# Optimization experiments

Measured on AMD Instinct MI355X. Metric: run time of the kernel, lower is better.

The kernel has to match this reference:

```python
import jax, jax.numpy as jnp
import numpy as np
import math

S, B, D = 1024, 8, 512
H = 8
HD = D // H
DFF = 2048
NUM_BUCKETS = 32
MAX_DISTANCE = 128
LN_EPS = 1e-5


def setup_inputs() -> dict:
    key = jax.random.key(0)
    ks = jax.random.split(key, 12)
    s = 0.02
    return {
        "x": jax.random.normal(ks[0], (S, B, D), jnp.float32),
        "attn_mask": jnp.zeros((S, S), jnp.float32),
        "in_proj_w": jax.random.normal(ks[1], (3 * D, D), jnp.float32) * s,
        "in_proj_b": jnp.zeros((3 * D,), jnp.float32),
        "out_proj_w": jax.random.normal(ks[2], (D, D), jnp.float32) * s,
        "out_proj_b": jnp.zeros((D,), jnp.float32),
        "lin1_w": jax.random.normal(ks[3], (DFF, D), jnp.float32) * s,
        "lin1_b": jnp.zeros((DFF,), jnp.float32),
        "lin2_w": jax.random.normal(ks[4], (D, DFF), jnp.float32) * s,
        "lin2_b": jnp.zeros((D,), jnp.float32),
        "ln1_w": jnp.ones((D,), jnp.float32),
        "ln1_b": jnp.zeros((D,), jnp.float32),
        "ln2_w": jnp.ones((D,), jnp.float32),
        "ln2_b": jnp.zeros((D,), jnp.float32),
        "rel_emb": jax.random.normal(ks[5], (NUM_BUCKETS, H), jnp.float32) * s,
    }


def _relative_position_bucket(relative_position, num_buckets=NUM_BUCKETS, max_distance=MAX_DISTANCE):
    # bidirectional=True path (encoder)
    nb = num_buckets // 2
    rel_buckets = (relative_position > 0).astype(jnp.int32) * nb
    rp = jnp.abs(relative_position)
    max_exact = nb // 2
    is_small = rp < max_exact
    rp_safe = jnp.maximum(rp, 1)  # avoid log(0); masked by is_small below
    rp_large = max_exact + (
        jnp.log(rp_safe.astype(jnp.float32) / max_exact)
        / math.log(max_distance / max_exact)
        * (nb - max_exact)
    ).astype(jnp.int32)
    rp_large = jnp.minimum(rp_large, nb - 1)
    return rel_buckets + jnp.where(is_small, rp, rp_large)


def _compute_bias(rel_emb, q_len, k_len):
    ctx = jnp.arange(q_len, dtype=jnp.int32)[:, None]
    mem = jnp.arange(k_len, dtype=jnp.int32)[None, :]
    buckets = _relative_position_bucket(mem - ctx)          # [S, S]
    values = rel_emb[buckets]                                # [S, S, H]
    return jnp.transpose(values, (2, 0, 1))                  # [H, S, S]


def _layer_norm(x, w, b):
    mu = jnp.mean(x, axis=-1, keepdims=True)
    var = jnp.mean(jnp.square(x - mu), axis=-1, keepdims=True)
    return (x - mu) * jax.lax.rsqrt(var + LN_EPS) * w + b


def reference(x, attn_mask, in_proj_w, in_proj_b, out_proj_w, out_proj_b,
              lin1_w, lin1_b, lin2_w, lin2_b, ln1_w, ln1_b, ln2_w, ln2_b, rel_emb):
    s, b, d = x.shape
    # qkv projection (torch Linear: y = x W^T + b)
    qkv = x @ in_proj_w.T + in_proj_b                         # [S, B, 3D]
    q, k, v = jnp.split(qkv, 3, axis=-1)

    def to_bhsd(t):
        return jnp.transpose(t.reshape(s, b, H, HD), (1, 2, 0, 3))  # [B, H, S, HD]

    q, k, v = to_bhsd(q), to_bhsd(k), to_bhsd(v)
    scores = jnp.einsum("bhqd,bhkd->bhqk", q, k) / math.sqrt(HD)

    bias = _compute_bias(rel_emb, s, s)                       # [H, S, S]
    mask_bias = attn_mask[None, :, :] + bias                  # [H, S, S]
    attn = jax.nn.softmax(scores + mask_bias[None], axis=-1)  # [B, H, S, S]

    o = jnp.einsum("bhqk,bhkd->bhqd", attn, v)                # [B, H, S, HD]
    o = jnp.transpose(o, (2, 0, 1, 3)).reshape(s, b, d)       # [S, B, D]
    o = o @ out_proj_w.T + out_proj_b

    # post-norm (norm_first=False)
    y = _layer_norm(x + o, ln1_w, ln1_b)
    ff = jax.nn.relu(y @ lin1_w.T + lin1_b) @ lin2_w.T + lin2_b
    return _layer_norm(y + ff, ln2_w, ln2_b)
```

## Files before the change

kernel.cpp:

```cpp
#include <hip/hip_runtime.h>
#include <hip/hip_bf16.h>


#define S_LEN 1024
#define BATCH 8
#define DMODEL 512
#define NHEAD 8
#define HDIM 64
#define DFF 2048
#define NROWS (S_LEN * BATCH)

typedef __bf16 bf16x8 __attribute__((ext_vector_type(8)));
typedef short  s16x4  __attribute__((ext_vector_type(4)));
typedef float  f32x4  __attribute__((ext_vector_type(4)));

__device__ __forceinline__ void gload16(const void* g, void* l) {
    __builtin_amdgcn_global_load_lds(
        (const __attribute__((address_space(1))) void*)g,
        (__attribute__((address_space(3))) void*)l, 16, 0, 0);
}

__global__ __launch_bounds__(256)
void prep_embc_kernel(const float* __restrict__ x,
                      const float* __restrict__ wq, const float* __restrict__ wo,
                      const float* __restrict__ w1, const float* __restrict__ w2,
                      __hip_bfloat16* __restrict__ xb, __hip_bfloat16* __restrict__ wqb,
                      __hip_bfloat16* __restrict__ wob, __hip_bfloat16* __restrict__ w1b,
                      __hip_bfloat16* __restrict__ w2b,
                      const float* __restrict__ mask,
                      const float* __restrict__ rel_emb,
                      __hip_bfloat16* __restrict__ embC) {
    if (blockIdx.x < 7168) {
        const int NX = NROWS * DMODEL / 4;
        const int NQ = 3 * DMODEL * DMODEL / 4;
        const int NO = DMODEL * DMODEL / 4;
        const int N1 = DFF * DMODEL / 4;
        int i = blockIdx.x * 256 + threadIdx.x;
        const float* src; __hip_bfloat16* dst; int off;
        if (i < NX)                         { src = x;  dst = xb;  off = i; }
        else if ((i -= NX) < NQ)            { src = wq; dst = wqb; off = i; }
        else if ((i -= NQ) < NO)            { src = wo; dst = wob; off = i; }
        else if ((i -= NO) < N1)            { src = w1; dst = w1b; off = i; }
        else if ((i -= N1) < N1)            { src = w2; dst = w2b; off = i; }
        else return;
        float4 v = *(const float4*)(src + (size_t)off * 4);
        union { s16x4 s; __hip_bfloat16 b[4]; } u;
        u.b[0] = __float2bfloat16(v.x); u.b[1] = __float2bfloat16(v.y);
        u.b[2] = __float2bfloat16(v.z); u.b[3] = __float2bfloat16(v.w);
        *(s16x4*)(dst + (size_t)off * 4) = u.s;
    } else {
        int tid = (blockIdx.x - 7168) * 256 + threadIdx.x;
        int h  = tid >> 16;
        int r1 = tid & 65535;
        int qt = r1 >> 12;
        int w  = (r1 >> 10) & 3;
        int kb = (r1 >> 6) & 15;
        int lane = r1 & 63;
        int q = qt * 64 + w * 16 + (lane & 15);
        __hip_bfloat16 ov[16];
#pragma unroll
        for (int j = 0; j < 16; ++j) {
            int c = j >> 2, e = j & 3;
            int k = kb * 64 + c * 16 + (lane >> 4) * 4 + e;
            int rel = k - q;
            int bucket = (rel > 0) ? 16 : 0;
            int rp = rel < 0 ? -rel : rel;
            int v;
            if (rp < 8)          v = rp;
            else if (rp < 12)    v = 8;
            else if (rp < 16)    v = 9;
            else if (rp < 23)    v = 10;
            else if (rp < 32)    v = 11;
            else if (rp < 46)    v = 12;
            else if (rp < 64)    v = 13;
            else if (rp < 91)    v = 14;
            else                 v = 15;
            float bt = rel_emb[(bucket + v) * NHEAD + h];
            ov[j] = __float2bfloat16(__expf(mask[(size_t)q * S_LEN + k] + bt));
        }
        *(uint4*)(embC + (size_t)tid * 16) = *(uint4*)&ov[0];
        *(uint4*)(embC + (size_t)tid * 16 + 8) = *(uint4*)&ov[8];
    }
}

template <int MODE, bool RELU>
__global__ __launch_bounds__(256)
void gemm_tile(const __hip_bfloat16* __restrict__ Ab,
               const __hip_bfloat16* __restrict__ Wb,
               const float* __restrict__ bias,
               void* __restrict__ outv,
               int N, int M, int Kloop, int Kstride) {
    const int id = blockIdx.x;
    int by, bx, bz;
    if (MODE == 0) { bz = id >> 8; int rem = id & 255; by = rem & 63; bx = rem >> 6; }
    else           { bz = 0; by = id & 63; bx = id >> 6; }
    const int w = threadIdx.x >> 6;
    const int lane = threadIdx.x & 63;
    const int m16 = lane & 15;
    const int quad = lane >> 4;
    const int row0 = by * 128;
    const int col0 = bx * 128;
    const int kbase = bz * Kloop;
    const int rowbase = (w >> 1) * 64;
    const int colbase = (w & 1) * 64;

    __shared__ __align__(16) __bf16 As[128 * 64];
    __shared__ __align__(16) __bf16 Bs[128 * 64];

    const __bf16* Ap = (const __bf16*)Ab;
    const __bf16* Wp = (const __bf16*)Wb;

    const int a_row_in_grp = lane >> 3;
    const int kb_sw = (lane & 7) ^ (lane >> 3);

    f32x4 acc[4][4];
#pragma unroll
    for (int c = 0; c < 4; ++c)
#pragma unroll
        for (int r = 0; r < 4; ++r) acc[c][r] = f32x4{0, 0, 0, 0};

    for (int k0 = 0; k0 < Kloop; k0 += 64) {
#pragma unroll
        for (int i = 0; i < 4; ++i) {
            int grp = w * 4 + i;
            int row = grp * 8 + a_row_in_grp;
            gload16(Ap + (size_t)(row0 + row) * Kstride + kbase + k0 + kb_sw * 8,
                    (void*)(As + grp * 512));
            gload16(Wp + (size_t)(col0 + row) * Kstride + kbase + k0 + kb_sw * 8,
                    (void*)(Bs + grp * 512));
        }
        __syncthreads();

#pragma unroll
        for (int kk = 0; kk < 2; ++kk) {
            bf16x8 af[4], bfr[4];
            int slot = (kk * 4 + quad) ^ (m16 & 7);
#pragma unroll
            for (int r = 0; r < 4; ++r)
                af[r] = *(const bf16x8*)(As + (rowbase + r * 16 + m16) * 64 + slot * 8);
#pragma unroll
            for (int c = 0; c < 4; ++c)
                bfr[c] = *(const bf16x8*)(Bs + (colbase + c * 16 + m16) * 64 + slot * 8);
#pragma unroll
            for (int c = 0; c < 4; ++c)
#pragma unroll
                for (int r = 0; r < 4; ++r)
                    acc[c][r] = __builtin_amdgcn_mfma_f32_16x16x32_bf16(
                        af[r], bfr[c], acc[c][r], 0, 0, 0);
        }
        __syncthreads();
    }

#pragma unroll
    for (int c = 0; c < 4; ++c) {
        int col = col0 + colbase + c * 16 + m16;
        float bv = (MODE == 0 && bz != 0) ? 0.f : bias[col];
#pragma unroll
        for (int r = 0; r < 4; ++r) {
#pragma unroll
            for (int e = 0; e < 4; ++e) {
                int row = row0 + rowbase + r * 16 + quad * 4 + e;
                float v = acc[c][r][e] + bv;
                if (RELU) v = fmaxf(v, 0.f);
                if (MODE == 0) {
                    ((float*)outv)[(size_t)bz * N * M + (size_t)row * M + col] = v;
                } else if (MODE == 1) {
                    ((__hip_bfloat16*)outv)[(size_t)row * M + col] = __float2bfloat16(v);
                } else {
                    int sect = col >> 9, h = (col >> 6) & 7, d = col & 63;
                    int s = row >> 3, bb = row & 7;
                    size_t idx;
                    if (sect == 2)
                        idx = (size_t)(128 + bb * 8 + h) * (S_LEN * HDIM)
                            + (size_t)d * S_LEN + s;
                    else
                        idx = ((size_t)(sect * 64 + bb * 8 + h) * S_LEN + s) * HDIM + d;
                    ((__hip_bfloat16*)outv)[idx] = __float2bfloat16(v);
                }
            }
        }
    }
}

__global__ __launch_bounds__(256)
void gemm64_db(const __hip_bfloat16* __restrict__ Ab,
               const __hip_bfloat16* __restrict__ Wb,
               const float* __restrict__ bias,
               float* __restrict__ outf,
               int N, int M, int K) {
    const int id = blockIdx.x;
    const int by = id & 63, bx = id >> 6;
    const int w = threadIdx.x >> 6;
    const int lane = threadIdx.x & 63;
    const int m16 = lane & 15;
    const int quad = lane >> 4;
    const int row0 = by * 128;
    const int col0 = bx * 64;
    const int rowbase = w * 32;

    __shared__ __align__(16) __bf16 As[2][128 * 64];
    __shared__ __align__(16) __bf16 Bs[2][64 * 64];

    const __bf16* Ap = (const __bf16*)Ab;
    const __bf16* Wp = (const __bf16*)Wb;

    const int a_row_in_grp = lane >> 3;
    const int kb_sw = (lane & 7) ^ (lane >> 3);

    auto stage = [&](int k0, int p) {
#pragma unroll
        for (int i = 0; i < 4; ++i) {
            int grp = w * 4 + i;
            int row = grp * 8 + a_row_in_grp;
            gload16(Ap + (size_t)(row0 + row) * K + k0 + kb_sw * 8,
                    (void*)(&As[p][grp * 512]));
        }
#pragma unroll
        for (int i = 0; i < 2; ++i) {
            int grp = w * 2 + i;
            int row = grp * 8 + a_row_in_grp;
            gload16(Wp + (size_t)(col0 + row) * K + k0 + kb_sw * 8,
                    (void*)(&Bs[p][grp * 512]));
        }
    };

    f32x4 acc[4][2];
#pragma unroll
    for (int c = 0; c < 4; ++c)
#pragma unroll
        for (int r = 0; r < 2; ++r) acc[c][r] = f32x4{0, 0, 0, 0};

    stage(0, 0);
    __syncthreads();

    int p = 0;
    for (int k0 = 0; k0 < K; k0 += 64, p ^= 1) {
        if (k0 + 64 < K) stage(k0 + 64, p ^ 1);
#pragma unroll
        for (int kk = 0; kk < 2; ++kk) {
            bf16x8 af[2], bfr[4];
            int slot = (kk * 4 + quad) ^ (m16 & 7);
#pragma unroll
            for (int r = 0; r < 2; ++r)
                af[r] = *(const bf16x8*)(&As[p][(rowbase + r * 16 + m16) * 64 + slot * 8]);
#pragma unroll
            for (int c = 0; c < 4; ++c)
                bfr[c] = *(const bf16x8*)(&Bs[p][(c * 16 + m16) * 64 + slot * 8]);
#pragma unroll
            for (int c = 0; c < 4; ++c)
#pragma unroll
                for (int r = 0; r < 2; ++r)
                    acc[c][r] = __builtin_amdgcn_mfma_f32_16x16x32_bf16(
                        af[r], bfr[c], acc[c][r], 0, 0, 0);
        }
        __syncthreads();
    }

#pragma unroll
    for (int c = 0; c < 4; ++c) {
        int col = col0 + c * 16 + m16;
        float bv = bias[col];
#pragma unroll
        for (int r = 0; r < 2; ++r)
#pragma unroll
            for (int e = 0; e < 4; ++e) {
                int row = row0 + rowbase + r * 16 + quad * 4 + e;
                outf[(size_t)row * M + col] = acc[c][r][e] + bv;
            }
    }
}

__global__ __launch_bounds__(256, 2)
void attn_mfma(const __hip_bfloat16* __restrict__ qkv_bhsd,
               const __hip_bfloat16* __restrict__ embC,
               __hip_bfloat16* __restrict__ o) {
    const int id = blockIdx.x;
    const int h = id & 7;
    const int qb = (id >> 3) & 7;
    const int b = id >> 6;
    const int bh = b * 8 + h;
    const int q0 = qb * 128;
    const int t = threadIdx.x;
    const int w = t >> 6, lane = t & 63, m16 = lane & 15, quad = lane >> 4;

    const __bf16* Qb  = (const __bf16*)qkv_bhsd + (size_t)bh * (S_LEN * HDIM);
    const __bf16* Kb  = (const __bf16*)qkv_bhsd + (size_t)(64 + bh) * (S_LEN * HDIM);
    const __bf16* VTg = (const __bf16*)qkv_bhsd + (size_t)(128 + bh) * (S_LEN * HDIM);
    const int qtA = qb * 2, qtB = qtA + 1;
    const __hip_bfloat16* ecA =
        embC + ((((size_t)h * 16 + qtA) * 4 + w) * 16) * 1024 + (size_t)lane * 16;
    const __hip_bfloat16* ecB =
        embC + ((((size_t)h * 16 + qtB) * 4 + w) * 16) * 1024 + (size_t)lane * 16;

    __shared__ __align__(16) __bf16 Ks[2][64 * 64];
    __shared__ __align__(16) __bf16 Vs[2][64 * 64];
    __shared__ __align__(16) __bf16 P[4][2][16 * 64];

    const int r_in = lane >> 3;
    const int kb_sw = (lane & 7) ^ r_in;

    auto stage = [&](int kc, int p) {
#pragma unroll
        for (int i = 0; i < 2; ++i) {
            int grp = w * 2 + i;
            gload16(Kb + (size_t)(kc + grp * 8 + r_in) * HDIM + kb_sw * 8,
                    (void*)(&Ks[p][grp * 512]));
            gload16(VTg + (size_t)(grp * 8 + r_in) * S_LEN + kc + kb_sw * 8,
                    (void*)(&Vs[p][grp * 512]));
        }
    };

    bf16x8 aQ0A, aQ1A, aQ0B, aQ1B;
    {
        const __bf16* qpA = Qb + (size_t)(q0 + w * 16 + m16) * HDIM + quad * 8;
        const __bf16* qpB = qpA + (size_t)64 * HDIM;
        bf16x8 t0 = *(const bf16x8*)qpA;
        bf16x8 t1 = *(const bf16x8*)(qpA + 32);
        bf16x8 t2 = *(const bf16x8*)qpB;
        bf16x8 t3 = *(const bf16x8*)(qpB + 32);
#pragma unroll
        for (int j = 0; j < 8; ++j) {
            t0[j] = (__bf16)((float)t0[j] * 0.125f);
            t1[j] = (__bf16)((float)t1[j] * 0.125f);
            t2[j] = (__bf16)((float)t2[j] * 0.125f);
            t3[j] = (__bf16)((float)t3[j] * 0.125f);
        }
        aQ0A = t0; aQ1A = t1; aQ0B = t2; aQ1B = t3;
    }

    f32x4 accOTA[4] = {f32x4{0,0,0,0}, f32x4{0,0,0,0}, f32x4{0,0,0,0}, f32x4{0,0,0,0}};
    f32x4 accOTB[4] = {f32x4{0,0,0,0}, f32x4{0,0,0,0}, f32x4{0,0,0,0}, f32x4{0,0,0,0}};
    float lpartA = 0.f, lpartB = 0.f;

    stage(0, 0);
    __syncthreads();

    int p = 0;
    for (int kc = 0; kc < S_LEN; kc += 64, p ^= 1) {
        if (kc + 64 < S_LEN) stage(kc + 64, p ^ 1);

        union { uint4 u[2]; __hip_bfloat16 e[16]; } evA, evB;
        evA.u[0] = *(const uint4*)(ecA + (size_t)(kc >> 6) * 1024);
        evA.u[1] = *(const uint4*)(ecA + (size_t)(kc >> 6) * 1024 + 8);
        evB.u[0] = *(const uint4*)(ecB + (size_t)(kc >> 6) * 1024);
        evB.u[1] = *(const uint4*)(ecB + (size_t)(kc >> 6) * 1024 + 8);

        f32x4 accTA[4] = {f32x4{0,0,0,0}, f32x4{0,0,0,0}, f32x4{0,0,0,0}, f32x4{0,0,0,0}};
        f32x4 accTB[4] = {f32x4{0,0,0,0}, f32x4{0,0,0,0}, f32x4{0,0,0,0}, f32x4{0,0,0,0}};
        const int sub = (m16 >> 3) * 512 + (m16 & 7) * 64;
        const int s0 = (quad ^ (m16 & 7)) * 8;
        const int s1 = ((4 + quad) ^ (m16 & 7)) * 8;
#pragma unroll
        for (int c = 0; c < 4; ++c) {
            const __bf16* kr = &Ks[p][c * 1024 + sub];
            bf16x8 b0 = *(const bf16x8*)(kr + s0);
            bf16x8 b1 = *(const bf16x8*)(kr + s1);
            accTA[c] = __builtin_amdgcn_mfma_f32_16x16x32_bf16(b0, aQ0A, accTA[c], 0, 0, 0);
            accTA[c] = __builtin_amdgcn_mfma_f32_16x16x32_bf16(b1, aQ1A, accTA[c], 0, 0, 0);
            accTB[c] = __builtin_amdgcn_mfma_f32_16x16x32_bf16(b0, aQ0B, accTB[c], 0, 0, 0);
            accTB[c] = __builtin_amdgcn_mfma_f32_16x16x32_bf16(b1, aQ1B, accTB[c], 0, 0, 0);
        }

#pragma unroll
        for (int c = 0; c < 4; ++c) {
            union { s16x4 s; __hip_bfloat16 bb[4]; } uA, uB;
#pragma unroll
            for (int e = 0; e < 4; ++e) {
                float pvA = __expf(accTA[c][e]) * __bfloat162float(evA.e[c * 4 + e]);
                float pvB = __expf(accTB[c][e]) * __bfloat162float(evB.e[c * 4 + e]);
                lpartA += pvA; lpartB += pvB;
                uA.bb[e] = __float2bfloat16(pvA);
                uB.bb[e] = __float2bfloat16(pvB);
            }
            int blk = (c * 2 + (quad >> 1)) ^ (m16 & 7);
            *(s16x4*)&P[w][0][m16 * 64 + blk * 8 + (quad & 1) * 4] = uA.s;
            *(s16x4*)&P[w][1][m16 * 64 + blk * 8 + (quad & 1) * 4] = uB.s;
        }

        bf16x8 pb0A = *(const bf16x8*)&P[w][0][m16 * 64 + ((quad) ^ (m16 & 7)) * 8];
        bf16x8 pb1A = *(const bf16x8*)&P[w][0][m16 * 64 + ((4 + quad) ^ (m16 & 7)) * 8];
        bf16x8 pb0B = *(const bf16x8*)&P[w][1][m16 * 64 + ((quad) ^ (m16 & 7)) * 8];
        bf16x8 pb1B = *(const bf16x8*)&P[w][1][m16 * 64 + ((4 + quad) ^ (m16 & 7)) * 8];

#pragma unroll
        for (int dt = 0; dt < 4; ++dt) {
            const __bf16* vr = &Vs[p][dt * 1024 + sub];
            bf16x8 v0 = *(const bf16x8*)(vr + s0);
            bf16x8 v1 = *(const bf16x8*)(vr + s1);
            accOTA[dt] = __builtin_amdgcn_mfma_f32_16x16x32_bf16(v0, pb0A, accOTA[dt], 0, 0, 0);
            accOTA[dt] = __builtin_amdgcn_mfma_f32_16x16x32_bf16(v1, pb1A, accOTA[dt], 0, 0, 0);
            accOTB[dt] = __builtin_amdgcn_mfma_f32_16x16x32_bf16(v0, pb0B, accOTB[dt], 0, 0, 0);
            accOTB[dt] = __builtin_amdgcn_mfma_f32_16x16x32_bf16(v1, pb1B, accOTB[dt], 0, 0, 0);
        }

        __syncthreads();
    }

    float lA = lpartA, lB = lpartB;
    lA += __shfl_xor(lA, 16); lA += __shfl_xor(lA, 32);
    lB += __shfl_xor(lB, 16); lB += __shfl_xor(lB, 32);
    float invA = 1.f / lA, invB = 1.f / lB;

    {
        int qA = q0 + w * 16 + m16;
        __hip_bfloat16* opA = o + ((size_t)qA * BATCH + b) * DMODEL + h * HDIM;
        __hip_bfloat16* opB = opA + (size_t)64 * BATCH * DMODEL;
#pragma unroll
        for (int dt = 0; dt < 4; ++dt) {
            union { s16x4 s; __hip_bfloat16 bb[4]; } uA, uB;
#pragma unroll
            for (int e = 0; e < 4; ++e) {
                uA.bb[e] = __float2bfloat16(accOTA[dt][e] * invA);
                uB.bb[e] = __float2bfloat16(accOTB[dt][e] * invB);
            }
            *(s16x4*)(opA + dt * 16 + quad * 4) = uA.s;
            *(s16x4*)(opB + dt * 16 + quad * 4) = uB.s;
        }
    }
}

__global__ __launch_bounds__(64)
void ln_kernel(const float* __restrict__ resid,
               const float* __restrict__ gin,
               const float* __restrict__ gin2,
               const float* __restrict__ w,
               const float* __restrict__ b,
               float* __restrict__ outf,
               __hip_bfloat16* __restrict__ outb) {
    const int row = blockIdx.x;
    const int lane = threadIdx.x;
    const float* rp = resid + (size_t)row * DMODEL;
    const float* gp = gin + (size_t)row * DMODEL;

    float4 v[2];
    float s = 0.f, s2 = 0.f;
#pragma unroll
    for (int i = 0; i < 2; ++i) {
        int d = i * 256 + lane * 4;
        float4 a = *(const float4*)(rp + d);
        float4 g = *(const float4*)(gp + d);
        a.x += g.x; a.y += g.y; a.z += g.z; a.w += g.w;
        if (gin2) {
            float4 g2 = *(const float4*)(gin2 + (size_t)row * DMODEL + d);
            a.x += g2.x; a.y += g2.y; a.z += g2.z; a.w += g2.w;
        }
        v[i] = a;
        s += a.x + a.y + a.z + a.w;
        s2 += a.x * a.x + a.y * a.y + a.z * a.z + a.w * a.w;
    }
#pragma unroll
    for (int off = 32; off; off >>= 1) {
        s  += __shfl_xor(s, off);
        s2 += __shfl_xor(s2, off);
    }
    float mu = s * (1.f / DMODEL);
    float var = s2 * (1.f / DMODEL) - mu * mu;
    float rs = rsqrtf(var + 1e-5f);
#pragma unroll
    for (int i = 0; i < 2; ++i) {
        int d = i * 256 + lane * 4;
        float4 wv = *(const float4*)(w + d);
        float4 bv = *(const float4*)(b + d);
        float4 y;
        y.x = (v[i].x - mu) * rs * wv.x + bv.x;
        y.y = (v[i].y - mu) * rs * wv.y + bv.y;
        y.z = (v[i].z - mu) * rs * wv.z + bv.z;
        y.w = (v[i].w - mu) * rs * wv.w + bv.w;
        *(float4*)(outf + (size_t)row * DMODEL + d) = y;
        if (outb) {
            union { s16x4 s4; __hip_bfloat16 e[4]; } u;
            u.e[0] = __float2bfloat16(y.x); u.e[1] = __float2bfloat16(y.y);
            u.e[2] = __float2bfloat16(y.z); u.e[3] = __float2bfloat16(y.w);
            *(s16x4*)(outb + (size_t)row * DMODEL + d) = u.s4;
        }
    }
}

extern "C" void kernel_launch(void* const* d_in, const int* in_sizes, int n_in,
                              void* d_out, int out_size, void* d_ws, size_t ws_size,
                              hipStream_t stream) {
    const float* x          = (const float*)d_in[0];
    const float* attn_mask  = (const float*)d_in[1];
    const float* in_proj_w  = (const float*)d_in[2];
    const float* in_proj_b  = (const float*)d_in[3];
    const float* out_proj_w = (const float*)d_in[4];
    const float* out_proj_b = (const float*)d_in[5];
    const float* lin1_w     = (const float*)d_in[6];
    const float* lin1_b     = (const float*)d_in[7];
    const float* lin2_w     = (const float*)d_in[8];
    const float* lin2_b     = (const float*)d_in[9];
    const float* ln1_w      = (const float*)d_in[10];
    const float* ln1_b      = (const float*)d_in[11];
    const float* ln2_w      = (const float*)d_in[12];
    const float* ln2_b      = (const float*)d_in[13];
    const float* rel_emb    = (const float*)d_in[14];

    char* ws = (char*)d_ws;
    size_t off = 0;
    auto alloc = [&](size_t bytes) {
        char* p = ws + off;
        off += (bytes + 255) / 256 * 256;
        return (void*)p;
    };
    __hip_bfloat16* embt  = (__hip_bfloat16*)alloc((size_t)NHEAD * S_LEN * S_LEN * 2);
    __hip_bfloat16* wqkvb = (__hip_bfloat16*)alloc((size_t)3 * DMODEL * DMODEL * 2);
    __hip_bfloat16* wob   = (__hip_bfloat16*)alloc((size_t)DMODEL * DMODEL * 2);
    __hip_bfloat16* w1b   = (__hip_bfloat16*)alloc((size_t)DFF * DMODEL * 2);
    __hip_bfloat16* w2b   = (__hip_bfloat16*)alloc((size_t)DMODEL * DFF * 2);
    __hip_bfloat16* xb    = (__hip_bfloat16*)alloc((size_t)NROWS * DMODEL * 2);
    __hip_bfloat16* qkvb  = (__hip_bfloat16*)alloc((size_t)3 * 64 * S_LEN * HDIM * 2);
    __hip_bfloat16* o     = (__hip_bfloat16*)alloc((size_t)NROWS * DMODEL * 2);
    float* tmp            = (float*)alloc((size_t)2 * NROWS * DMODEL * 4);
    float* yf             = (float*)alloc((size_t)NROWS * DMODEL * 4);
    __hip_bfloat16* yb    = (__hip_bfloat16*)alloc((size_t)NROWS * DMODEL * 2);
    __hip_bfloat16* ffb   = (__hip_bfloat16*)alloc((size_t)NROWS * DFF * 2);

    float* out = (float*)d_out;
    float* tmp2 = tmp + (size_t)NROWS * DMODEL;

    prep_embc_kernel<<<dim3(9216), 256, 0, stream>>>(
        x, in_proj_w, out_proj_w, lin1_w, lin2_w, xb, wqkvb, wob, w1b, w2b,
        attn_mask, rel_emb, embt);

    gemm_tile<2, false><<<dim3(768), 256, 0, stream>>>(
        xb, wqkvb, in_proj_b, qkvb, NROWS, 3 * DMODEL, DMODEL, DMODEL);

    attn_mfma<<<dim3(512), 256, 0, stream>>>(qkvb, embt, o);

    gemm64_db<<<dim3(512), 256, 0, stream>>>(
        o, wob, out_proj_b, tmp, NROWS, DMODEL, DMODEL);

    ln_kernel<<<dim3(NROWS), 64, 0, stream>>>(x, tmp, nullptr, ln1_w, ln1_b, yf, yb);

    gemm_tile<1, true><<<dim3(1024), 256, 0, stream>>>(
        yb, w1b, lin1_b, ffb, NROWS, DFF, DMODEL, DMODEL);

    gemm_tile<0, false><<<dim3(512), 256, 0, stream>>>(
        ffb, w2b, lin2_b, tmp, NROWS, DMODEL, DFF / 2, DFF);

    ln_kernel<<<dim3(NROWS), 64, 0, stream>>>(yf, tmp, tmp2, ln2_w, ln2_b, out, nullptr);
}
```

Measured before the change: 267.7 us.

## Add 256x256-tile double-buffered GEMM for QKV and FFN1 projections

```diff
diff --git a/kernel.cpp b/kernel.cpp
--- a/kernel.cpp
+++ b/kernel.cpp
@@ -84,6 +84,140 @@
 }
 
 template <int MODE, bool RELU>
+__global__ __launch_bounds__(512, 2)
+void gemm256(const __hip_bfloat16* __restrict__ Ab,
+             const __hip_bfloat16* __restrict__ Wb,
+             const float* __restrict__ bias,
+             void* __restrict__ outv,
+             int M, int K) {
+    const int id = blockIdx.x;
+    const int by = id & 31;
+    const int bx = id >> 5;
+    const int w = threadIdx.x >> 6;
+    const int lane = threadIdx.x & 63;
+    const int m16 = lane & 15;
+    const int quad = lane >> 4;
+    const int wr = w >> 2;
+    const int wc = w & 3;
+    const int row0 = by * 256;
+    const int col0 = bx * 256;
+
+    __shared__ __align__(16) __bf16 As[2][256 * 64];
+    __shared__ __align__(16) __bf16 Bs[2][256 * 64];
+
+    const __bf16* Ap = (const __bf16*)Ab;
+    const __bf16* Wp = (const __bf16*)Wb;
+
+    const int r_in = lane >> 3;
+    const int kb_sw = (lane & 7) ^ r_in;
+
+    auto stageAh = [&](int k0, int hf, int p) {
+#pragma unroll
+        for (int i = 0; i < 2; ++i) {
+            int grp = w * 2 + i;
+            int row = hf * 128 + grp * 8 + r_in;
+            gload16(Ap + (size_t)(row0 + row) * K + k0 + kb_sw * 8,
+                    (void*)(&As[p][(hf * 128 + grp * 8) * 64]));
+        }
+    };
+    auto stageBh = [&](int k0, int hf, int p) {
+#pragma unroll
+        for (int i = 0; i < 2; ++i) {
+            int grp = w * 2 + i;
+            int row = hf * 128 + grp * 8 + r_in;
+            gload16(Wp + (size_t)(col0 + row) * K + k0 + kb_sw * 8,
+                    (void*)(&Bs[p][(hf * 128 + grp * 8) * 64]));
+        }
+    };
+
+    f32x4 acc[8][4];
+#pragma unroll
+    for (int mi = 0; mi < 8; ++mi)
+#pragma unroll
+        for (int ni = 0; ni < 4; ++ni) acc[mi][ni] = f32x4{0, 0, 0, 0};
+
+    const int NT = K / 64;
+
+    stageAh(0, 0, 0); stageAh(0, 1, 0);
+    stageBh(0, 0, 0); stageBh(0, 1, 0);
+    asm volatile("s_waitcnt vmcnt(0)" ::: "memory");
+    __builtin_amdgcn_s_barrier();
+
+    for (int t = 0; t < NT; ++t) {
+        const int p = t & 1;
+        const int kn = (t + 1) * 64;
+        const bool pf = (t + 1 < NT);
+#pragma unroll
+        for (int q = 0; q < 4; ++q) {
+            if (q == 0 && pf) { stageAh(kn, 0, p ^ 1); stageAh(kn, 1, p ^ 1); }
+            if (q == 1 && pf) { stageBh(kn, 0, p ^ 1); stageBh(kn, 1, p ^ 1); }
+
+            const int mh = q >> 1, nh = q & 1;
+            bf16x8 af[2][4], bfr[2][2];
+#pragma unroll
+            for (int kk = 0; kk < 2; ++kk) {
+                const int slot = (kk * 4 + quad) ^ (m16 & 7);
+#pragma unroll
+                for (int r = 0; r < 4; ++r) {
+                    int row = wr * 128 + mh * 64 + r * 16 + m16;
+                    af[kk][r] = *(const bf16x8*)(&As[p][row * 64 + slot * 8]);
+                }
+#pragma unroll
+                for (int c = 0; c < 2; ++c) {
+                    int col = wc * 64 + nh * 32 + c * 16 + m16;
+                    bfr[kk][c] = *(const bf16x8*)(&Bs[p][col * 64 + slot * 8]);
+                }
+            }
+
+            __builtin_amdgcn_s_barrier();
+
+            __builtin_amdgcn_s_setprio(1);
+#pragma unroll
+            for (int kk = 0; kk < 2; ++kk)
+#pragma unroll
+                for (int c = 0; c < 2; ++c)
+#pragma unroll
+                    for (int r = 0; r < 4; ++r)
+                        acc[mh * 4 + r][nh * 2 + c] =
+                            __builtin_amdgcn_mfma_f32_16x16x32_bf16(
+                                af[kk][r], bfr[kk][c], acc[mh * 4 + r][nh * 2 + c],
+                                0, 0, 0);
+            __builtin_amdgcn_s_setprio(0);
+        }
+        if (pf) asm volatile("s_waitcnt vmcnt(0)" ::: "memory");
+        __builtin_amdgcn_s_barrier();
+    }
+
+#pragma unroll
+    for (int ni = 0; ni < 4; ++ni) {
+        int col = col0 + wc * 64 + ni * 16 + m16;
+        float bv = bias[col];
+#pragma unroll
+        for (int mi = 0; mi < 8; ++mi) {
+#pragma unroll
+            for (int e = 0; e < 4; ++e) {
+                int row = row0 + wr * 128 + mi * 16 + quad * 4 + e;
+                float v = acc[mi][ni][e] + bv;
+                if (RELU) v = fmaxf(v, 0.f);
+                if (MODE == 1) {
+                    ((__hip_bfloat16*)outv)[(size_t)row * M + col] = __float2bfloat16(v);
+                } else {
+                    int sect = col >> 9, h = (col >> 6) & 7, d = col & 63;
+                    int s = row >> 3, bb = row & 7;
+                    size_t idx;
+                    if (sect == 2)
+                        idx = (size_t)(128 + bb * 8 + h) * (S_LEN * HDIM)
+                            + (size_t)d * S_LEN + s;
+                    else
+                        idx = ((size_t)(sect * 64 + bb * 8 + h) * S_LEN + s) * HDIM + d;
+                    ((__hip_bfloat16*)outv)[idx] = __float2bfloat16(v);
+                }
+            }
+        }
+    }
+}
+
+template <int MODE, bool RELU>
 __global__ __launch_bounds__(256)
 void gemm_tile(const __hip_bfloat16* __restrict__ Ab,
                const __hip_bfloat16* __restrict__ Wb,
@@ -522,8 +656,8 @@
         x, in_proj_w, out_proj_w, lin1_w, lin2_w, xb, wqkvb, wob, w1b, w2b,
         attn_mask, rel_emb, embt);
 
-    gemm_tile<2, false><<<dim3(768), 256, 0, stream>>>(
-        xb, wqkvb, in_proj_b, qkvb, NROWS, 3 * DMODEL, DMODEL, DMODEL);
+    gemm256<2, false><<<dim3(192), 512, 0, stream>>>(
+        xb, wqkvb, in_proj_b, qkvb, 3 * DMODEL, DMODEL);
 
     attn_mfma<<<dim3(512), 256, 0, stream>>>(qkvb, embt, o);
 
@@ -532,8 +666,8 @@
 
     ln_kernel<<<dim3(NROWS), 64, 0, stream>>>(x, tmp, nullptr, ln1_w, ln1_b, yf, yb);
 
-    gemm_tile<1, true><<<dim3(1024), 256, 0, stream>>>(
-        yb, w1b, lin1_b, ffb, NROWS, DFF, DMODEL, DMODEL);
+    gemm256<1, true><<<dim3(256), 512, 0, stream>>>(
+        yb, w1b, lin1_b, ffb, DFF, DMODEL);
 
     gemm_tile<0, false><<<dim3(512), 256, 0, stream>>>(
         ffb, w2b, lin2_b, tmp, NROWS, DMODEL, DFF / 2, DFF);
```

New measurement: 295.8 us. 1.1x slower.
